# Kernel tuning notes

Hardware: AMD Instinct MI355X
Metric: run time of the kernel (lower is better)

## Reference

```python
import jax, jax.numpy as jnp
import numpy as np

B, T, H, NB, D, DH = 2, 8192, 16, 32, 1024, 128


def setup_inputs() -> dict:
    key = jax.random.key(0)
    ks = jax.random.split(key, 4)
    theta_path = jax.random.normal(ks[0], (B, T, H, NB), dtype=jnp.float32)
    content_emb = jax.random.normal(ks[1], (B, T, D), dtype=jnp.float32)
    W1 = jax.random.normal(ks[2], (D, DH), dtype=jnp.float32) / np.sqrt(D)
    b1 = jnp.zeros((DH,), dtype=jnp.float32)
    W2 = jax.random.normal(ks[3], (DH, H * NB), dtype=jnp.float32) / np.sqrt(DH)
    b2 = jnp.zeros((H * NB,), dtype=jnp.float32)
    log_Q = jnp.full((H, NB), -3.0, dtype=jnp.float32)  # torch init: full(-3.0)
    log_R = jnp.full((H, NB), 1.0, dtype=jnp.float32)   # torch init: full(1.0)
    return {"theta_path": theta_path, "content_emb": content_emb,
            "W1": W1, "b1": b1, "W2": W2, "b2": b2,
            "log_Q": log_Q, "log_R": log_R}


def _steady_state_K(log_Q, log_R):
    # closed-form scalar DARE: K* = (P+Q)/(P+Q+R), P = (-Q + sqrt(Q^2+4QR))/2
    Q = jnp.exp(log_Q)
    R = jnp.exp(log_R)
    P_post = 0.5 * (-Q + jnp.sqrt(Q * Q + 4.0 * Q * R))
    P_pred = P_post + Q
    return P_pred / (P_pred + R)


def _parallel_affine_scan(nu, K_star):
    # d_t = K * sum_{s<=t} (1-K)^(t-s) nu_s via zero-padded FFT convolution
    b, t, h, nb = nu.shape
    alpha = 1.0 - K_star                                   # (H, NB)
    k_idx = jnp.arange(t, dtype=nu.dtype)
    kernel = K_star[..., None] * (alpha[..., None] ** k_idx)  # (H, NB, T)
    pad_len = 2 * t
    kernel_fft = jnp.fft.rfft(kernel, n=pad_len, axis=-1)     # (H, NB, pad/2+1)
    nu_perm = jnp.transpose(nu, (0, 2, 3, 1))                 # (B, H, NB, T)
    nu_fft = jnp.fft.rfft(nu_perm, n=pad_len, axis=-1)
    conv = jnp.fft.irfft(nu_fft * kernel_fft[None], n=pad_len, axis=-1)[..., :t]
    return jnp.transpose(conv, (0, 3, 1, 2))                  # (B, T, H, NB)


def reference(theta_path, content_emb, W1, b1, W2, b2, log_Q, log_R):
    b, t, h, nb = theta_path.shape
    hid = jax.nn.gelu(content_emb @ W1 + b1, approximate=False)  # exact GELU (torch default)
    z_raw = (hid @ W2 + b2).reshape(b, t, h, nb)
    z = jnp.pi * jnp.tanh(z_raw)
    diff = z - theta_path
    nu = jnp.arctan2(jnp.sin(diff), jnp.cos(diff))  # wrap to (-pi, pi]
    K_star = _steady_state_K(log_Q, log_R)
    d = _parallel_affine_scan(nu, K_star)
    theta_hat = theta_path + d
    return theta_hat, d, K_star
```

## Files before the change

### kernel.cpp

```cpp
#include <hip/hip_runtime.h>
#include <math.h>

#define Bq 2
#define Tq 8192
#define Dq 1024
#define DHq 128
#define HNq 512
#define Mq (Bq*Tq)
#define NELEM ((size_t)Mq*HNq)
#define CHL 16
#define NCHK (Mq/CHL)
#define CPS (Tq/CHL)

typedef _Float16 half8 __attribute__((ext_vector_type(8)));
typedef float    f32x4 __attribute__((ext_vector_type(4)));

#define SC_LO  2048.0f
#define ISC_LO 4.8828125e-4f

__device__ __forceinline__ float gelu_exact(float x) {
    return 0.5f * x * (1.0f + erff(x * 0.7071067811865475f));
}

__device__ __forceinline__ float wrap_pi(float d) {
    return fmaf(-6.283185307179586f, rintf(d * 0.15915494309189535f), d);
}

__global__ __launch_bounds__(64) void p0_pack(
    const float* __restrict__ W1, const float* __restrict__ W2,
    const float* __restrict__ lq, const float* __restrict__ lr,
    _Float16* __restrict__ w1h, _Float16* __restrict__ w1l,
    _Float16* __restrict__ w2h, _Float16* __restrict__ w2l,
    float* __restrict__ Karr, float* __restrict__ Aarr,
    float* __restrict__ kout)
{
    const int l = threadIdx.x;
    const int u = blockIdx.x;
    if (u == 384) {
        #pragma unroll
        for (int i = 0; i < 8; ++i) {
            int col = i * 64 + l;
            float Q = expf(lq[col]);
            float R = expf(lr[col]);
            float P = 0.5f * (-Q + sqrtf(fmaf(Q, Q, 4.0f * Q * R)));
            float Pp = P + Q;
            float K = Pp / (Pp + R);
            Karr[col] = K;
            Aarr[col] = 1.0f - K;
            kout[col] = K;
        }
        return;
    }
    const float* W; _Float16 *ph, *pl; int ncols, kt, ct, unit;
    if (u < 256) { unit = u;       kt = unit >> 3; ct = unit & 7;  W = W1; ph = w1h; pl = w1l; ncols = 128; }
    else         { unit = u - 256; kt = unit >> 5; ct = unit & 31; W = W2; ph = w2h; pl = w2l; ncols = 512; }
    const int col = ct * 16 + (l & 15);
    const int k0  = kt * 32 + ((l >> 4) * 8);
    half8 hv, lv;
    #pragma unroll
    for (int j = 0; j < 8; ++j) {
        float x = W[(size_t)(k0 + j) * ncols + col];
        _Float16 h = (_Float16)x;
        hv[j] = h;
        lv[j] = (_Float16)((x - (float)h) * SC_LO);
    }
    size_t off = ((size_t)unit * 64 + l) * 8;
    *(half8*)(ph + off) = hv;
    *(half8*)(pl + off) = lv;
}

__global__ __launch_bounds__(512) void k1_mfma(
    const float* __restrict__ A, const _Float16* __restrict__ w1h,
    const _Float16* __restrict__ w1l, const float* __restrict__ b1,
    _Float16* __restrict__ hidH, _Float16* __restrict__ hidL)
{
    __shared__ float ldsR[64][132];
    const int tid = threadIdx.x;
    const int w = tid >> 6, l = tid & 63;
    const int lrow = l & 15, lq = l >> 4;
    const int rt = w & 3, kh = w >> 2;
    const int rm = blockIdx.x * 64;

    f32x4 accM[8] = {};
    f32x4 accC[8] = {};
    const float* ap = A + (size_t)(rm + rt * 16 + lrow) * Dq + kh * 512 + lq * 8;

    for (int step = 0; step < 16; ++step) {
        f32x4 x0 = *(const f32x4*)(ap);
        f32x4 x1 = *(const f32x4*)(ap + 4);
        ap += 32;
        half8 ah, alo;
        float xs[8] = {x0[0], x0[1], x0[2], x0[3], x1[0], x1[1], x1[2], x1[3]};
        #pragma unroll
        for (int j = 0; j < 8; ++j) {
            _Float16 h = (_Float16)xs[j];
            ah[j]  = h;
            alo[j] = (_Float16)((xs[j] - (float)h) * SC_LO);
        }
        const int ktG = kh * 16 + step;
        #pragma unroll
        for (int ct = 0; ct < 8; ++ct) {
            size_t boff = ((size_t)(ktG * 8 + ct) * 64 + l) * 8;
            const half8 bh = *(const half8*)(w1h + boff);
            const half8 bl = *(const half8*)(w1l + boff);
            accM[ct] = __builtin_amdgcn_mfma_f32_16x16x32_f16(ah,  bh, accM[ct], 0, 0, 0);
            accC[ct] = __builtin_amdgcn_mfma_f32_16x16x32_f16(ah,  bl, accC[ct], 0, 0, 0);
            accC[ct] = __builtin_amdgcn_mfma_f32_16x16x32_f16(alo, bh, accC[ct], 0, 0, 0);
        }
    }

    if (kh == 0) {
        #pragma unroll
        for (int ct = 0; ct < 8; ++ct)
            #pragma unroll
            for (int r = 0; r < 4; ++r)
                ldsR[rt * 16 + lq * 4 + r][ct * 16 + lrow] =
                    fmaf(accC[ct][r], ISC_LO, accM[ct][r]);
    }
    __syncthreads();
    if (kh == 1) {
        #pragma unroll
        for (int ct = 0; ct < 8; ++ct)
            #pragma unroll
            for (int r = 0; r < 4; ++r)
                ldsR[rt * 16 + lq * 4 + r][ct * 16 + lrow] +=
                    fmaf(accC[ct][r], ISC_LO, accM[ct][r]);
    }
    __syncthreads();

    const int mt = w & 3;
    const int ktb = (w >> 2) * 2;
    #pragma unroll
    for (int kk = 0; kk < 2; ++kk) {
        const int kt = ktb + kk;
        const int dh0 = kt * 32 + lq * 8;
        const float* rp = &ldsR[mt * 16 + lrow][dh0];
        f32x4 s0 = *(const f32x4*)rp;
        f32x4 s1 = *(const f32x4*)(rp + 4);
        f32x4 bb0 = *(const f32x4*)(b1 + dh0);
        f32x4 bb1 = *(const f32x4*)(b1 + dh0 + 4);
        half8 hv, lv;
        #pragma unroll
        for (int j = 0; j < 4; ++j) {
            float g = gelu_exact(s0[j] + bb0[j]);
            _Float16 h = (_Float16)g;
            hv[j] = h; lv[j] = (_Float16)((g - (float)h) * SC_LO);
        }
        #pragma unroll
        for (int j = 0; j < 4; ++j) {
            float g = gelu_exact(s1[j] + bb1[j]);
            _Float16 h = (_Float16)g;
            hv[4 + j] = h; lv[4 + j] = (_Float16)((g - (float)h) * SC_LO);
        }
        size_t off = (((size_t)(blockIdx.x * 4 + mt) * 4 + kt) * 64 + l) * 8;
        *(half8*)(hidH + off) = hv;
        *(half8*)(hidL + off) = lv;
    }
}

__global__ __launch_bounds__(256, 4) void k2a_mfma(
    const _Float16* __restrict__ hidH, const _Float16* __restrict__ hidL,
    const _Float16* __restrict__ w2h, const _Float16* __restrict__ w2l,
    const float* __restrict__ b2, const float* __restrict__ theta,
    const float* __restrict__ Karr, const float* __restrict__ Aarr,
    float* __restrict__ nuG, float* __restrict__ carries)
{
    __shared__ float nuL[16][516];
    const int tid = threadIdx.x;
    const int w = tid >> 6, l = tid & 63;
    const int lrow = l & 15, lq = l >> 4;
    const int blk = blockIdx.x;

    f32x4 accM[8] = {};
    f32x4 accC[8] = {};
    #pragma unroll
    for (int kt = 0; kt < 4; ++kt) {
        size_t aoff = (((size_t)blk * 4 + kt) * 64 + l) * 8;
        const half8 ah  = *(const half8*)(hidH + aoff);
        const half8 alo = *(const half8*)(hidL + aoff);
        #pragma unroll
        for (int ct = 0; ct < 8; ++ct) {
            const int ctG = w * 8 + ct;
            size_t boff = (((size_t)kt * 32 + ctG) * 64 + l) * 8;
            const half8 bh = *(const half8*)(w2h + boff);
            const half8 bl = *(const half8*)(w2l + boff);
            accM[ct] = __builtin_amdgcn_mfma_f32_16x16x32_f16(ah,  bh, accM[ct], 0, 0, 0);
            accC[ct] = __builtin_amdgcn_mfma_f32_16x16x32_f16(ah,  bl, accC[ct], 0, 0, 0);
            accC[ct] = __builtin_amdgcn_mfma_f32_16x16x32_f16(alo, bh, accC[ct], 0, 0, 0);
        }
    }

    const float PI_F = 3.14159265358979323846f;
    #pragma unroll
    for (int ct = 0; ct < 8; ++ct) {
        const int col = w * 128 + ct * 16 + lrow;
        const float bb = b2[col];
        #pragma unroll
        for (int r = 0; r < 4; ++r) {
            const int row = blk * 16 + lq * 4 + r;
            float z = fmaf(accC[ct][r], ISC_LO, accM[ct][r]) + bb;
            float t = PI_F * tanhf(z);
            size_t io = (size_t)row * HNq + col;
            accM[ct][r] = wrap_pi(t - theta[io]);
        }
    }
    #pragma unroll
    for (int ct = 0; ct < 8; ++ct)
        #pragma unroll
        for (int r = 0; r < 4; ++r)
            nuL[lq * 4 + r][w * 128 + ct * 16 + lrow] = accM[ct][r];
    __syncthreads();

    #pragma unroll
    for (int cc = 0; cc < 2; ++cc) {
        const int col = tid + cc * 256;
        const float K = Karr[col], al = Aarr[col];
        float c = 0.0f;
        #pragma unroll
        for (int r = 0; r < 16; ++r)
            c = fmaf(al, c, K * nuL[r][col]);
        carries[(size_t)blk * HNq + col] = c;
    }
    f32x4* dst = (f32x4*)nuG + (size_t)blk * 2048;
    #pragma unroll
    for (int it = 0; it < 8; ++it) {
        const int g = tid + it * 256;
        const int row = g >> 7, cw = g & 127;
        dst[g] = *(const f32x4*)&nuL[row][cw * 4];
    }
}

__global__ __launch_bounds__(256) void k2b_scan(
    const float* __restrict__ theta, const float* __restrict__ Karr,
    const float* __restrict__ Aarr, const float* __restrict__ carries,
    float* __restrict__ nud, float* __restrict__ theta_hat)
{
    const int tid = threadIdx.x;
    const int sub = tid >> 7, cg = tid & 127, c0 = cg * 4;
    const int chunk = blockIdx.x * 2 + sub;
    const int cloc = chunk & (CPS - 1);
    const int seq0 = chunk - cloc;

    const f32x4 K4 = *(const f32x4*)(Karr + c0);
    const f32x4 A4 = *(const f32x4*)(Aarr + c0);
    f32x4 A16;
    #pragma unroll
    for (int j = 0; j < 4; ++j) {
        float a2 = A4[j] * A4[j];
        float a4 = a2 * a2;
        float a8 = a4 * a4;
        A16[j] = a8 * a8;
    }
    float amax = fmaxf(fmaxf(A16[0], A16[1]), fmaxf(A16[2], A16[3]));
    int n = cloc;
    if (amax <= 0.0f) {
        n = 0;
    } else {
        float ln = logf(amax);
        if (ln < -1e-6f) {
            int nn = (int)ceilf(-33.0f / ln);
            if (nn < n) n = nn;
        }
    }
    f32x4 s = {0.0f, 0.0f, 0.0f, 0.0f};
    for (int j = cloc - n; j < cloc; ++j) {
        f32x4 cv = *(const f32x4*)(carries + (size_t)(seq0 + j) * HNq + c0);
        s = A16 * s + cv;
    }

    const size_t base = (size_t)chunk * CHL * HNq + c0;
    #pragma unroll 4
    for (int r = 0; r < CHL; ++r) {
        const size_t idx = base + (size_t)r * HNq;
        f32x4 nu = *(const f32x4*)(nud + idx);
        f32x4 th = *(const f32x4*)(theta + idx);
        s = A4 * s + K4 * nu;
        *(f32x4*)(nud + idx) = s;
        *(f32x4*)(theta_hat + idx) = th + s;
    }
}

extern "C" void kernel_launch(void* const* d_in, const int* in_sizes, int n_in,
                              void* d_out, int out_size, void* d_ws, size_t ws_size,
                              hipStream_t stream) {
    const float* theta   = (const float*)d_in[0];
    const float* content = (const float*)d_in[1];
    const float* W1      = (const float*)d_in[2];
    const float* b1      = (const float*)d_in[3];
    const float* W2      = (const float*)d_in[4];
    const float* b2      = (const float*)d_in[5];
    const float* logQ    = (const float*)d_in[6];
    const float* logR    = (const float*)d_in[7];

    float* out       = (float*)d_out;
    float* theta_hat = out;
    float* dbuf      = out + NELEM;
    float* kout      = out + 2 * NELEM;

    _Float16* w1h  = (_Float16*)d_ws;
    _Float16* w1l  = w1h + 131072;
    _Float16* w2h  = w1l + 131072;
    _Float16* w2l  = w2h + 65536;
    _Float16* hidH = w2l + 65536;
    _Float16* hidL = hidH + 2097152;
    float* Karr    = (float*)(hidL + 2097152);
    float* Aarr    = Karr + 512;
    float* carries = Aarr + 512;

    p0_pack<<<dim3(385), 64, 0, stream>>>(W1, W2, logQ, logR,
                                          w1h, w1l, w2h, w2l, Karr, Aarr, kout);
    k1_mfma<<<dim3(Mq / 64), 512, 0, stream>>>(content, w1h, w1l, b1, hidH, hidL);
    k2a_mfma<<<dim3(NCHK), 256, 0, stream>>>(hidH, hidL, w2h, w2l, b2, theta,
                                             Karr, Aarr, dbuf, carries);
    k2b_scan<<<dim3(NCHK / 2), 256, 0, stream>>>(theta, Karr, Aarr, carries,
                                                 dbuf, theta_hat);
}
```

Measured before the change: 238.1 us.

## Shrink k1 tiles with register prefetch and halve scan chunk length

k1 now processes 16 rows per 256-thread block instead of 64 rows per 512 threads. Each wave computes half the output columns for one K half, and the next A slice is prefetched into registers while the current one is split and multiplied. The scan chunk drops from 16 to 8 rows, so k2a emits two carries per 16-row tile and k2b launches twice as many blocks, each with a shorter serial loop but more carry terms to fold. The aim is more parallelism and latency hiding, traded for more W1 reloads across blocks and a larger carries buffer.

```diff
diff --git a/kernel.cpp b/kernel.cpp
--- a/kernel.cpp
+++ b/kernel.cpp
@@ -10,13 +10,16 @@
 #define NELEM ((size_t)Mq*HNq)
 #define CHL 16
 #define NCHK (Mq/CHL)
-#define CPS (Tq/CHL)
+#define CH8 8
+#define NC8 (Mq/CH8)
+#define CPS8 (Tq/CH8)
 
 typedef _Float16 half8 __attribute__((ext_vector_type(8)));
 typedef float    f32x4 __attribute__((ext_vector_type(4)));
 
 #define SC_LO  2048.0f
 #define ISC_LO 4.8828125e-4f
+
 
 __device__ __forceinline__ float gelu_exact(float x) {
     return 0.5f * x * (1.0f + erff(x * 0.7071067811865475f));
@@ -69,93 +72,101 @@
     *(half8*)(pl + off) = lv;
 }
 
-__global__ __launch_bounds__(512) void k1_mfma(
+__global__ __launch_bounds__(256, 4) void k1_mfma(
     const float* __restrict__ A, const _Float16* __restrict__ w1h,
     const _Float16* __restrict__ w1l, const float* __restrict__ b1,
     _Float16* __restrict__ hidH, _Float16* __restrict__ hidL)
 {
-    __shared__ float ldsR[64][132];
+    __shared__ float ldsR[16 * 132];
     const int tid = threadIdx.x;
     const int w = tid >> 6, l = tid & 63;
     const int lrow = l & 15, lq = l >> 4;
-    const int rt = w & 3, kh = w >> 2;
-    const int rm = blockIdx.x * 64;
-
-    f32x4 accM[8] = {};
-    f32x4 accC[8] = {};
-    const float* ap = A + (size_t)(rm + rt * 16 + lrow) * Dq + kh * 512 + lq * 8;
+    const int kh = w >> 1, ns = w & 1;
+    const int row = blockIdx.x * 16 + lrow;
+
+    f32x4 accM[4] = {};
+    f32x4 accC[4] = {};
+    const float* ap = A + (size_t)row * Dq + kh * 512 + lq * 8;
+
+    f32x4 a0 = *(const f32x4*)(ap);
+    f32x4 a1 = *(const f32x4*)(ap + 4);
 
     for (int step = 0; step < 16; ++step) {
-        f32x4 x0 = *(const f32x4*)(ap);
-        f32x4 x1 = *(const f32x4*)(ap + 4);
-        ap += 32;
+        f32x4 n0, n1;
+        if (step < 15) {
+            n0 = *(const f32x4*)(ap + (step + 1) * 32);
+            n1 = *(const f32x4*)(ap + (step + 1) * 32 + 4);
+        }
         half8 ah, alo;
-        float xs[8] = {x0[0], x0[1], x0[2], x0[3], x1[0], x1[1], x1[2], x1[3]};
-        #pragma unroll
-        for (int j = 0; j < 8; ++j) {
-            _Float16 h = (_Float16)xs[j];
-            ah[j]  = h;
-            alo[j] = (_Float16)((xs[j] - (float)h) * SC_LO);
+        {
+            float xs[8] = {a0[0], a0[1], a0[2], a0[3], a1[0], a1[1], a1[2], a1[3]};
+            #pragma unroll
+            for (int j = 0; j < 8; ++j) {
+                _Float16 h = (_Float16)xs[j];
+                ah[j]  = h;
+                alo[j] = (_Float16)((xs[j] - (float)h) * SC_LO);
+            }
         }
         const int ktG = kh * 16 + step;
         #pragma unroll
-        for (int ct = 0; ct < 8; ++ct) {
-            size_t boff = ((size_t)(ktG * 8 + ct) * 64 + l) * 8;
+        for (int ct = 0; ct < 4; ++ct) {
+            const int ctG = ns * 4 + ct;
+            size_t boff = ((size_t)(ktG * 8 + ctG) * 64 + l) * 8;
             const half8 bh = *(const half8*)(w1h + boff);
             const half8 bl = *(const half8*)(w1l + boff);
             accM[ct] = __builtin_amdgcn_mfma_f32_16x16x32_f16(ah,  bh, accM[ct], 0, 0, 0);
             accC[ct] = __builtin_amdgcn_mfma_f32_16x16x32_f16(ah,  bl, accC[ct], 0, 0, 0);
             accC[ct] = __builtin_amdgcn_mfma_f32_16x16x32_f16(alo, bh, accC[ct], 0, 0, 0);
         }
+        a0 = n0; a1 = n1;
     }
 
     if (kh == 0) {
         #pragma unroll
-        for (int ct = 0; ct < 8; ++ct)
+        for (int ct = 0; ct < 4; ++ct) {
+            const int ctG = ns * 4 + ct;
             #pragma unroll
             for (int r = 0; r < 4; ++r)
-                ldsR[rt * 16 + lq * 4 + r][ct * 16 + lrow] =
+                ldsR[(lq * 4 + r) * 132 + ctG * 16 + lrow] =
                     fmaf(accC[ct][r], ISC_LO, accM[ct][r]);
+        }
     }
     __syncthreads();
     if (kh == 1) {
         #pragma unroll
-        for (int ct = 0; ct < 8; ++ct)
+        for (int ct = 0; ct < 4; ++ct) {
+            const int ctG = ns * 4 + ct;
             #pragma unroll
             for (int r = 0; r < 4; ++r)
-                ldsR[rt * 16 + lq * 4 + r][ct * 16 + lrow] +=
+                ldsR[(lq * 4 + r) * 132 + ctG * 16 + lrow] +=
                     fmaf(accC[ct][r], ISC_LO, accM[ct][r]);
+        }
     }
     __syncthreads();
 
-    const int mt = w & 3;
-    const int ktb = (w >> 2) * 2;
-    #pragma unroll
-    for (int kk = 0; kk < 2; ++kk) {
-        const int kt = ktb + kk;
-        const int dh0 = kt * 32 + lq * 8;
-        const float* rp = &ldsR[mt * 16 + lrow][dh0];
-        f32x4 s0 = *(const f32x4*)rp;
-        f32x4 s1 = *(const f32x4*)(rp + 4);
-        f32x4 bb0 = *(const f32x4*)(b1 + dh0);
-        f32x4 bb1 = *(const f32x4*)(b1 + dh0 + 4);
-        half8 hv, lv;
-        #pragma unroll
-        for (int j = 0; j < 4; ++j) {
-            float g = gelu_exact(s0[j] + bb0[j]);
-            _Float16 h = (_Float16)g;
-            hv[j] = h; lv[j] = (_Float16)((g - (float)h) * SC_LO);
-        }
-        #pragma unroll
-        for (int j = 0; j < 4; ++j) {
-            float g = gelu_exact(s1[j] + bb1[j]);
-            _Float16 h = (_Float16)g;
-            hv[4 + j] = h; lv[4 + j] = (_Float16)((g - (float)h) * SC_LO);
-        }
-        size_t off = (((size_t)(blockIdx.x * 4 + mt) * 4 + kt) * 64 + l) * 8;
-        *(half8*)(hidH + off) = hv;
-        *(half8*)(hidL + off) = lv;
-    }
+    const int kt = w;
+    const int dh0 = kt * 32 + lq * 8;
+    const float* rp = ldsR + lrow * 132 + dh0;
+    f32x4 s0 = *(const f32x4*)rp;
+    f32x4 s1 = *(const f32x4*)(rp + 4);
+    f32x4 bb0 = *(const f32x4*)(b1 + dh0);
+    f32x4 bb1 = *(const f32x4*)(b1 + dh0 + 4);
+    half8 hv, lv;
+    #pragma unroll
+    for (int j = 0; j < 4; ++j) {
+        float g = gelu_exact(s0[j] + bb0[j]);
+        _Float16 h = (_Float16)g;
+        hv[j] = h; lv[j] = (_Float16)((g - (float)h) * SC_LO);
+    }
+    #pragma unroll
+    for (int j = 0; j < 4; ++j) {
+        float g = gelu_exact(s1[j] + bb1[j]);
+        _Float16 h = (_Float16)g;
+        hv[4 + j] = h; lv[4 + j] = (_Float16)((g - (float)h) * SC_LO);
+    }
+    size_t off = (((size_t)blockIdx.x * 4 + kt) * 64 + l) * 8;
+    *(half8*)(hidH + off) = hv;
+    *(half8*)(hidL + off) = lv;
 }
 
 __global__ __launch_bounds__(256, 4) void k2a_mfma(
@@ -163,7 +174,7 @@
     const _Float16* __restrict__ w2h, const _Float16* __restrict__ w2l,
     const float* __restrict__ b2, const float* __restrict__ theta,
     const float* __restrict__ Karr, const float* __restrict__ Aarr,
-    float* __restrict__ nuG, float* __restrict__ carries)
+    float* __restrict__ nuG, float* __restrict__ carries8)
 {
     __shared__ float nuL[16][516];
     const int tid = threadIdx.x;
@@ -215,11 +226,14 @@
     for (int cc = 0; cc < 2; ++cc) {
         const int col = tid + cc * 256;
         const float K = Karr[col], al = Aarr[col];
-        float c = 0.0f;
-        #pragma unroll
-        for (int r = 0; r < 16; ++r)
-            c = fmaf(al, c, K * nuL[r][col]);
-        carries[(size_t)blk * HNq + col] = c;
+        #pragma unroll
+        for (int sub = 0; sub < 2; ++sub) {
+            float c = 0.0f;
+            #pragma unroll
+            for (int r = 0; r < 8; ++r)
+                c = fmaf(al, c, K * nuL[sub * 8 + r][col]);
+            carries8[(size_t)(blk * 2 + sub) * HNq + col] = c;
+        }
     }
     f32x4* dst = (f32x4*)nuG + (size_t)blk * 2048;
     #pragma unroll
@@ -232,45 +246,44 @@
 
 __global__ __launch_bounds__(256) void k2b_scan(
     const float* __restrict__ theta, const float* __restrict__ Karr,
-    const float* __restrict__ Aarr, const float* __restrict__ carries,
+    const float* __restrict__ Aarr, const float* __restrict__ carries8,
     float* __restrict__ nud, float* __restrict__ theta_hat)
 {
     const int tid = threadIdx.x;
     const int sub = tid >> 7, cg = tid & 127, c0 = cg * 4;
     const int chunk = blockIdx.x * 2 + sub;
-    const int cloc = chunk & (CPS - 1);
+    const int cloc = chunk & (CPS8 - 1);
     const int seq0 = chunk - cloc;
 
     const f32x4 K4 = *(const f32x4*)(Karr + c0);
     const f32x4 A4 = *(const f32x4*)(Aarr + c0);
-    f32x4 A16;
+    f32x4 A8;
     #pragma unroll
     for (int j = 0; j < 4; ++j) {
         float a2 = A4[j] * A4[j];
         float a4 = a2 * a2;
-        float a8 = a4 * a4;
-        A16[j] = a8 * a8;
-    }
-    float amax = fmaxf(fmaxf(A16[0], A16[1]), fmaxf(A16[2], A16[3]));
+        A8[j] = a4 * a4;
+    }
+    float amax = fmaxf(fmaxf(A8[0], A8[1]), fmaxf(A8[2], A8[3]));
     int n = cloc;
     if (amax <= 0.0f) {
         n = 0;
     } else {
         float ln = logf(amax);
-        if (ln < -1e-6f) {
-            int nn = (int)ceilf(-33.0f / ln);
+        if (ln < -1e-9f) {
+            int nn = (int)ceilf(-34.0f / ln);
             if (nn < n) n = nn;
         }
     }
     f32x4 s = {0.0f, 0.0f, 0.0f, 0.0f};
     for (int j = cloc - n; j < cloc; ++j) {
-        f32x4 cv = *(const f32x4*)(carries + (size_t)(seq0 + j) * HNq + c0);
-        s = A16 * s + cv;
-    }
-
-    const size_t base = (size_t)chunk * CHL * HNq + c0;
-    #pragma unroll 4
-    for (int r = 0; r < CHL; ++r) {
+        f32x4 cv = *(const f32x4*)(carries8 + (size_t)(seq0 + j) * HNq + c0);
+        s = A8 * s + cv;
+    }
+
+    const size_t base = (size_t)chunk * CH8 * HNq + c0;
+    #pragma unroll
+    for (int r = 0; r < CH8; ++r) {
         const size_t idx = base + (size_t)r * HNq;
         f32x4 nu = *(const f32x4*)(nud + idx);
         f32x4 th = *(const f32x4*)(theta + idx);
@@ -305,13 +318,13 @@
     _Float16* hidL = hidH + 2097152;
     float* Karr    = (float*)(hidL + 2097152);
     float* Aarr    = Karr + 512;
-    float* carries = Aarr + 512;
+    float* carries8 = Aarr + 512;
 
     p0_pack<<<dim3(385), 64, 0, stream>>>(W1, W2, logQ, logR,
                                           w1h, w1l, w2h, w2l, Karr, Aarr, kout);
-    k1_mfma<<<dim3(Mq / 64), 512, 0, stream>>>(content, w1h, w1l, b1, hidH, hidL);
+    k1_mfma<<<dim3(Mq / 16), 256, 0, stream>>>(content, w1h, w1l, b1, hidH, hidL);
     k2a_mfma<<<dim3(NCHK), 256, 0, stream>>>(hidH, hidL, w2h, w2l, b2, theta,
-                                             Karr, Aarr, dbuf, carries);
-    k2b_scan<<<dim3(NCHK / 2), 256, 0, stream>>>(theta, Karr, Aarr, carries,
-                                                 dbuf, theta_hat);
-}
+                                             Karr, Aarr, dbuf, carries8);
+    k2b_scan<<<dim3(NC8 / 2), 256, 0, stream>>>(theta, Karr, Aarr, carries8,
+                                                dbuf, theta_hat);
+}
```

Result: faster. 223.7 us (-6.0%).
